# Kernel optimization log

Measured on AMD Instinct MI355X. Metric: run time of the kernel, lower is better.

The kernel has to match this reference:

```python
import jax, jax.numpy as jnp
import numpy as np

B, S = 64, 256
VOCAB, DL, DA, DV = 30522, 300, 74, 35
DH, GH, LH, RH = 128, 64, 128, 128  # modality dim, proj-GRU hidden, LSTM hidden, RGN hidden


def _gru_dir(x, Wi, Wh, bi, bh):
    # x: [B,S,D] -> [B,S,H]; torch GRU gate order (r, z, n)
    xg = x @ Wi + bi  # [B,S,3H] precomputed input projections
    H = Wh.shape[0]
    def step(h, xg_t):
        hg = h @ Wh + bh
        xr, xz, xn = jnp.split(xg_t, 3, axis=-1)
        hr, hz, hn = jnp.split(hg, 3, axis=-1)
        r = jax.nn.sigmoid(xr + hr)
        z = jax.nn.sigmoid(xz + hz)
        n = jnp.tanh(xn + r * hn)
        h = (1.0 - z) * n + z * h
        return h, h
    h0 = jnp.zeros((x.shape[0], H), x.dtype)
    _, ys = jax.lax.scan(step, h0, jnp.swapaxes(xg, 0, 1))
    return jnp.swapaxes(ys, 0, 1)


def _bigru(x, Wi, Wh, bi, bh):
    f = _gru_dir(x, Wi[0], Wh[0], bi[0], bh[0])
    b = _gru_dir(x[:, ::-1], Wi[1], Wh[1], bi[1], bh[1])[:, ::-1]
    return jnp.concatenate([f, b], axis=-1)


def _lstm_dir(x, Wi, Wh, bi, bh):
    xg = x @ Wi + bi  # [B,S,4H]; torch LSTM gate order (i, f, g, o)
    H = Wh.shape[0]
    def step(carry, xg_t):
        h, c = carry
        g = xg_t + h @ Wh + bh
        i, f, gg, o = jnp.split(g, 4, axis=-1)
        c = jax.nn.sigmoid(f) * c + jax.nn.sigmoid(i) * jnp.tanh(gg)
        h = jax.nn.sigmoid(o) * jnp.tanh(c)
        return (h, c), h
    z = jnp.zeros((x.shape[0], H), x.dtype)
    _, ys = jax.lax.scan(step, (z, z), jnp.swapaxes(xg, 0, 1))
    return jnp.swapaxes(ys, 0, 1)


def _bilstm(x, Wi, Wh, bi, bh):
    f = _lstm_dir(x, Wi[0], Wh[0], bi[0], bh[0])
    b = _lstm_dir(x[:, ::-1], Wi[1], Wh[1], bi[1], bh[1])[:, ::-1]
    return jnp.concatenate([f, b], axis=-1)


def _rgn_scan(x, h0, Wx, Wh, b):
    # RGNCell: gated recurrent cell (GRU-style), returns final state [B,H]
    xg = x @ Wx + b  # [B,S,3H]
    def step(h, xg_t):
        hg = h @ Wh
        xr, xz, xn = jnp.split(xg_t, 3, axis=-1)
        hr, hz, hn = jnp.split(hg, 3, axis=-1)
        r = jax.nn.sigmoid(xr + hr)
        z = jax.nn.sigmoid(xz + hz)
        n = jnp.tanh(xn + r * hn)
        return (1.0 - z) * n + z * h, None
    h, _ = jax.lax.scan(step, h0, jnp.swapaxes(xg, 0, 1))
    return h


def _xattn(q, kv):
    # parameter-free scaled dot-product cross-modal attention (JCAF)
    scale = 1.0 / np.sqrt(q.shape[-1]).astype(np.float32)
    s = jnp.einsum('bsd,btd->bst', q, kv) * scale
    return jnp.einsum('bst,btd->bsd', jax.nn.softmax(s, axis=-1), kv)


def _forward(sentences, acoustic, video, state0, state1, emb,
             proj_l_W, proj_l_b, proj_a_W, proj_a_b, proj_v_W, proj_v_b,
             gru_Wi, gru_Wh, gru_bi, gru_bh,
             lstm_Wi, lstm_Wh, lstm_bi, lstm_bh,
             rgn_Wx, rgn_Wh, rgn_b, fc1_W, fc1_b, fc2_W, fc2_b):
    enc = emb[sentences]                          # LanguageEmbeddingLayer: [B,S,DL]
    # SeqEncoder: project each modality to 128-d (dropout off in eval)
    seq_l = enc @ proj_l_W + proj_l_b             # [B,S,128]
    seq_a = acoustic @ proj_a_W + proj_a_b
    seq_v = video @ proj_v_W + proj_v_b
    # project_l/a/v: bidirectional GRU 128 -> 2*64 = 128
    x_l = _bigru(seq_l, gru_Wi[0], gru_Wh[0], gru_bi[0], gru_bh[0])
    x_a = _bigru(seq_a, gru_Wi[1], gru_Wh[1], gru_bi[1], gru_bh[1])
    x_v = _bigru(seq_v, gru_Wi[2], gru_Wh[2], gru_bi[2], gru_bh[2])
    # JCAF: each modality enriched by cross-attention to the other two
    fin_txt = x_l + _xattn(x_l, x_a) + _xattn(x_l, x_v)
    fin_aud = x_a + _xattn(x_a, x_l) + _xattn(x_a, x_v)
    fin_vis = x_v + _xattn(x_v, x_l) + _xattn(x_v, x_a)
    tstep = jnp.concatenate([fin_txt, fin_aud, fin_vis], axis=-1)      # [B,S,384]
    step_fusion = _bilstm(tstep, lstm_Wi, lstm_Wh, lstm_bi, lstm_bh)   # [B,S,256]
    # two custom RGNCell recurrences: forward sweep + reversed sweep
    out0 = _rgn_scan(step_fusion, state0, rgn_Wx[0], rgn_Wh[0], rgn_b[0])
    out1 = _rgn_scan(step_fusion[:, ::-1], state1, rgn_Wx[1], rgn_Wh[1], rgn_b[1])
    h = jax.nn.leaky_relu((out0 + out1) @ fc1_W + fc1_b)
    return h @ fc2_W + fc2_b                     # [B,1]


def setup_inputs():
    keys = iter(jax.random.split(jax.random.key(0), 48))
    def rn(shape, s=0.05):
        return jax.random.normal(next(keys), shape, jnp.float32) * s
    return {
        'sentences': jax.random.randint(next(keys), (B, S), 0, VOCAB),
        'acoustic': jax.random.normal(next(keys), (B, S, DA), jnp.float32),
        'video': jax.random.normal(next(keys), (B, S, DV), jnp.float32),
        'state0': jax.random.normal(next(keys), (B, RH), jnp.float32),
        'state1': jax.random.normal(next(keys), (B, RH), jnp.float32),
        'emb': rn((VOCAB, DL), 0.1),
        'proj_l_W': rn((DL, DH)), 'proj_l_b': rn((DH,)),
        'proj_a_W': rn((DA, DH)), 'proj_a_b': rn((DH,)),
        'proj_v_W': rn((DV, DH)), 'proj_v_b': rn((DH,)),
        'gru_Wi': rn((3, 2, DH, 3 * GH)), 'gru_Wh': rn((3, 2, GH, 3 * GH)),
        'gru_bi': rn((3, 2, 3 * GH)), 'gru_bh': rn((3, 2, 3 * GH)),
        'lstm_Wi': rn((2, 3 * DH, 4 * LH)), 'lstm_Wh': rn((2, LH, 4 * LH)),
        'lstm_bi': rn((2, 4 * LH)), 'lstm_bh': rn((2, 4 * LH)),
        'rgn_Wx': rn((2, 2 * LH, 3 * RH)), 'rgn_Wh': rn((2, RH, 3 * RH)),
        'rgn_b': rn((2, 3 * RH)),
        'fc1_W': rn((RH, 32)), 'fc1_b': rn((32,)),
        'fc2_W': rn((32, 1)), 'fc2_b': rn((1,)),
    }


def reference(sentences, acoustic, video, state0, state1, emb,
              proj_l_W, proj_l_b, proj_a_W, proj_a_b, proj_v_W, proj_v_b,
              gru_Wi, gru_Wh, gru_bi, gru_bh,
              lstm_Wi, lstm_Wh, lstm_bi, lstm_bh,
              rgn_Wx, rgn_Wh, rgn_b, fc1_W, fc1_b, fc2_W, fc2_b):
    return _forward(sentences, acoustic, video, state0, state1, emb,
                    proj_l_W, proj_l_b, proj_a_W, proj_a_b, proj_v_W, proj_v_b,
                    gru_Wi, gru_Wh, gru_bi, gru_bh,
                    lstm_Wi, lstm_Wh, lstm_bi, lstm_bh,
                    rgn_Wx, rgn_Wh, rgn_b, fc1_W, fc1_b, fc2_W, fc2_b)
```

## Files before the change

### kernel.cpp

```cpp
#include <hip/hip_runtime.h>

#define WS_SEQ      0LL
#define WS_XGGRU    6291456LL
#define WS_X        0LL
#define WS_TSTEP    18874368LL
#define WS_S        6291456LL
#define WS_XGLSTM   0LL
#define WS_SF       16777216LL
#define WS_XGRGN    0LL
#define WS_OUT0     20971520LL

__device__ __forceinline__ float sigf(float x) {
    return __builtin_amdgcn_rcpf(1.f + __expf(-x));
}
__device__ __forceinline__ float tanhfast(float x) {
    float e = __expf(2.f * x);
    return 1.f - 2.f * __builtin_amdgcn_rcpf(e + 1.f);
}

typedef float vf2 __attribute__((ext_vector_type(2)));

#define LDW64(W, P, S) { _Pragma("unroll") \
    for (int _k = 0; _k < 64; ++_k) (W)[_k] = *(const vf2*)((P) + _k * (S)); }

#define PK4(A0, A1, Wa, Wb, Wc, Wd, H, K0, K1, K2, K3) \
  asm("v_readlane_b32 s60, %6, " #K0 "\n\t" \
      "v_readlane_b32 s62, %6, " #K1 "\n\t" \
      "v_readlane_b32 s64, %6, " #K2 "\n\t" \
      "v_readlane_b32 s66, %6, " #K3 "\n\t" \
      "s_mov_b32 s61, s60\n\t" \
      "s_mov_b32 s63, s62\n\t" \
      "s_mov_b32 s65, s64\n\t" \
      "s_mov_b32 s67, s66\n\t" \
      "v_pk_fma_f32 %0, %2, s[60:61], %0\n\t" \
      "v_pk_fma_f32 %1, %3, s[62:63], %1\n\t" \
      "v_pk_fma_f32 %0, %4, s[64:65], %0\n\t" \
      "v_pk_fma_f32 %1, %5, s[66:67], %1" \
      : "+v"(A0), "+v"(A1) \
      : "v"(Wa), "v"(Wb), "v"(Wc), "v"(Wd), "v"(H) \
      : "s60","s61","s62","s63","s64","s65","s66","s67");

#define PKALL(A0, A1, W, H) \
  PK4(A0,A1,W[0],W[1],W[2],W[3],H,0,1,2,3) \
  PK4(A0,A1,W[4],W[5],W[6],W[7],H,4,5,6,7) \
  PK4(A0,A1,W[8],W[9],W[10],W[11],H,8,9,10,11) \
  PK4(A0,A1,W[12],W[13],W[14],W[15],H,12,13,14,15) \
  PK4(A0,A1,W[16],W[17],W[18],W[19],H,16,17,18,19) \
  PK4(A0,A1,W[20],W[21],W[22],W[23],H,20,21,22,23) \
  PK4(A0,A1,W[24],W[25],W[26],W[27],H,24,25,26,27) \
  PK4(A0,A1,W[28],W[29],W[30],W[31],H,28,29,30,31) \
  PK4(A0,A1,W[32],W[33],W[34],W[35],H,32,33,34,35) \
  PK4(A0,A1,W[36],W[37],W[38],W[39],H,36,37,38,39) \
  PK4(A0,A1,W[40],W[41],W[42],W[43],H,40,41,42,43) \
  PK4(A0,A1,W[44],W[45],W[46],W[47],H,44,45,46,47) \
  PK4(A0,A1,W[48],W[49],W[50],W[51],H,48,49,50,51) \
  PK4(A0,A1,W[52],W[53],W[54],W[55],H,52,53,54,55) \
  PK4(A0,A1,W[56],W[57],W[58],W[59],H,56,57,58,59) \
  PK4(A0,A1,W[60],W[61],W[62],W[63],H,60,61,62,63)

__device__ __forceinline__ void gemm_body(
    const float* __restrict__ Ab, int lda, const int* __restrict__ idx,
    const float* __restrict__ Wb, int wld, int wtrans,
    const float* __restrict__ bb,
    float* __restrict__ Cb, int ldc,
    int K, float alpha, int accum)
{
    int m0 = blockIdx.y * 64, n0 = blockIdx.x * 64;
    int t = threadIdx.x;
    int tx = t & 7, ty = t >> 3;

    __shared__ __align__(16) float As[16][68];
    __shared__ __align__(16) float Ws[16][68];

    float acc[8][8];
#pragma unroll
    for (int i = 0; i < 8; ++i)
#pragma unroll
        for (int j = 0; j < 8; ++j) acc[i][j] = 0.f;

    long long arow[4];
#pragma unroll
    for (int i = 0; i < 4; ++i) {
        int m = (t + i * 64) >> 2;
        arow[i] = idx ? (long long)idx[m0 + m] : (long long)(m0 + m);
    }
    const bool a_vec = ((lda & 3) == 0);

    for (int k0 = 0; k0 < K; k0 += 16) {
#pragma unroll
        for (int i = 0; i < 4; ++i) {
            int j = t + i * 64;
            int m = j >> 2, kq = j & 3;
            int kk = k0 + kq * 4;
            const float* p = Ab + arow[i] * (long long)lda + kk;
            float4 v = {0.f, 0.f, 0.f, 0.f};
            if (a_vec && kk + 3 < K) {
                v = *(const float4*)p;
            } else {
                if (kk + 0 < K) v.x = p[0];
                if (kk + 1 < K) v.y = p[1];
                if (kk + 2 < K) v.z = p[2];
                if (kk + 3 < K) v.w = p[3];
            }
            As[kq * 4 + 0][m] = v.x; As[kq * 4 + 1][m] = v.y;
            As[kq * 4 + 2][m] = v.z; As[kq * 4 + 3][m] = v.w;
        }
        if (!wtrans) {
#pragma unroll
            for (int i = 0; i < 4; ++i) {
                int j = t + i * 64;
                int k = j >> 4, nq = j & 15;
                float4 v = {0.f, 0.f, 0.f, 0.f};
                if (k0 + k < K)
                    v = *(const float4*)(Wb + (long long)(k0 + k) * wld + n0 + nq * 4);
                *(float4*)&Ws[k][nq * 4] = v;
            }
        } else {
#pragma unroll
            for (int i = 0; i < 4; ++i) {
                int j = t + i * 64;
                int n = j >> 2, kq = j & 3;
                int kk = k0 + kq * 4;
                const float* p = Wb + (long long)(n0 + n) * wld + kk;
                float4 v = {0.f, 0.f, 0.f, 0.f};
                if (kk + 3 < K) v = *(const float4*)p;
                else {
                    if (kk + 0 < K) v.x = p[0];
                    if (kk + 1 < K) v.y = p[1];
                    if (kk + 2 < K) v.z = p[2];
                    if (kk + 3 < K) v.w = p[3];
                }
                Ws[kq * 4 + 0][n] = v.x; Ws[kq * 4 + 1][n] = v.y;
                Ws[kq * 4 + 2][n] = v.z; Ws[kq * 4 + 3][n] = v.w;
            }
        }
        __syncthreads();
#pragma unroll
        for (int k = 0; k < 16; ++k) {
            float4 a0 = *(const float4*)&As[k][ty * 8];
            float4 a1 = *(const float4*)&As[k][ty * 8 + 4];
            float4 b0 = *(const float4*)&Ws[k][tx * 8];
            float4 b1 = *(const float4*)&Ws[k][tx * 8 + 4];
            float av[8] = {a0.x, a0.y, a0.z, a0.w, a1.x, a1.y, a1.z, a1.w};
            float bv[8] = {b0.x, b0.y, b0.z, b0.w, b1.x, b1.y, b1.z, b1.w};
#pragma unroll
            for (int i = 0; i < 8; ++i)
#pragma unroll
                for (int j = 0; j < 8; ++j)
                    acc[i][j] = fmaf(av[i], bv[j], acc[i][j]);
        }
        __syncthreads();
    }

#pragma unroll
    for (int i = 0; i < 8; ++i) {
        long long gm = m0 + ty * 8 + i;
#pragma unroll
        for (int jq = 0; jq < 2; ++jq) {
            float* cp = Cb + gm * ldc + n0 + tx * 8 + jq * 4;
            float4 v;
            v.x = alpha * acc[i][jq * 4 + 0]; v.y = alpha * acc[i][jq * 4 + 1];
            v.z = alpha * acc[i][jq * 4 + 2]; v.w = alpha * acc[i][jq * 4 + 3];
            if (bb) {
                const float* bp = bb + n0 + tx * 8 + jq * 4;
                v.x += bp[0]; v.y += bp[1]; v.z += bp[2]; v.w += bp[3];
            }
            if (accum) {
                float4 o = *(const float4*)cp;
                v.x += o.x; v.y += o.y; v.z += o.z; v.w += o.w;
            }
            *(float4*)cp = v;
        }
    }
}

__global__ __launch_bounds__(64) void gemm_k(
    const float* __restrict__ A, long long a_z, int a_zdiv, int lda,
    const int* __restrict__ idx,
    const float* __restrict__ W, long long w_z, int wld, int wtrans,
    const float* __restrict__ bias, int bias_z,
    float* __restrict__ C, long long c_z, int ldc,
    int K, float alpha, int accum)
{
    int z = blockIdx.z;
    gemm_body(A + (long long)(z / a_zdiv) * a_z, lda, idx,
              W + (long long)z * w_z, wld, wtrans,
              bias ? bias + (long long)z * bias_z : nullptr,
              C + (long long)z * c_z, ldc, K, alpha, accum);
}

__global__ __launch_bounds__(64) void att_score_k(
    const float* __restrict__ X, float* __restrict__ S,
    int q0, int q1, int q2, int k0, int k1, int k2)
{
    int z = blockIdx.z;
    int pair = z >> 6, b = z & 63;
    int qi = pair == 0 ? q0 : (pair == 1 ? q1 : q2);
    int ki = pair == 0 ? k0 : (pair == 1 ? k1 : k2);
    gemm_body(X + (long long)qi * 2097152 + (long long)b * 32768, 128, nullptr,
              X + (long long)ki * 2097152 + (long long)b * 32768, 128, 1,
              nullptr,
              S + (long long)z * 65536, 256, 128, 0.08838834764831845f, 0);
}

__global__ __launch_bounds__(64) void att_apply_k(
    const float* __restrict__ S, const float* __restrict__ X,
    float* __restrict__ tstep,
    int q0, int q1, int q2, int k0, int k1, int k2)
{
    int z = blockIdx.z;
    int pair = z >> 6, b = z & 63;
    int qi = pair == 0 ? q0 : (pair == 1 ? q1 : q2);
    int ki = pair == 0 ? k0 : (pair == 1 ? k1 : k2);
    gemm_body(S + (long long)z * 65536, 256, nullptr,
              X + (long long)ki * 2097152 + (long long)b * 32768, 128, 0,
              nullptr,
              tstep + (long long)qi * 128 + (long long)b * 98304, 384,
              256, 1.f, 1);
}

__global__ __launch_bounds__(256) void copy_tstep_k(const float* __restrict__ x,
                                                    float* __restrict__ tstep)
{
    int o = blockIdx.x * 256 + threadIdx.x;
    int c = o % 384;
    int row = o / 384;
    int m = c >> 7, cc = c & 127;
    tstep[o] = x[(long long)m * 2097152 + (long long)row * 128 + cc];
}

__global__ __launch_bounds__(256) void softmax_k(float* __restrict__ S)
{
    int wave = threadIdx.x >> 6, lane = threadIdx.x & 63;
    int row = blockIdx.x * 4 + wave;
    float* p = S + (long long)row * 256;
    float v[4];
    float mx = -1e30f;
#pragma unroll
    for (int i = 0; i < 4; ++i) { v[i] = p[lane + i * 64]; mx = fmaxf(mx, v[i]); }
#pragma unroll
    for (int off = 32; off > 0; off >>= 1) mx = fmaxf(mx, __shfl_xor(mx, off));
    float sum = 0.f;
#pragma unroll
    for (int i = 0; i < 4; ++i) { v[i] = __expf(v[i] - mx); sum += v[i]; }
#pragma unroll
    for (int off = 32; off > 0; off >>= 1) sum += __shfl_xor(sum, off);
    float inv = 1.f / sum;
#pragma unroll
    for (int i = 0; i < 4; ++i) p[lane + i * 64] = v[i] * inv;
}

__global__ __launch_bounds__(128) void gru_rec_k(const float* __restrict__ xg,
                                                 const float* __restrict__ Wh,
                                                 const float* __restrict__ bh,
                                                 float* __restrict__ xout)
{
    int b = blockIdx.x, z = blockIdx.y;
    int m = z >> 1, d = z & 1;
    int tid = threadIdx.x, lane = tid & 63;
    int cp = tid;
    int act = cp < 96;
    int cpc = act ? cp : 0;
    const float* Whz = Wh + (long long)z * 12288;
    const float* wp = Whz + 2 * cpc;
    vf2 Wk[64];
    LDW64(Wk, wp, 192);
    vf2 bias2 = *(const vf2*)(bh + z * 192 + 2 * cpc);

    __shared__ float g[2][192];
    int n = lane;
    float h = 0.f;
    const float* xgb = xg + (long long)z * 3145728 + (long long)b * 49152;
    float* xob = xout + (long long)m * 2097152 + (long long)b * 32768 + d * 64;
    int tt0 = d ? 255 : 0;
    const float* xr0 = xgb + tt0 * 192;
    float x_r = xr0[n], x_z = xr0[64 + n], x_n = xr0[128 + n];

#pragma unroll 1
    for (int t = 0; t < 256; ++t) {
        int tt = d ? 255 - t : t;
        float nx_r = 0, nx_z = 0, nx_n = 0;
        if (t < 255) {
            const float* xr = xgb + (d ? tt - 1 : tt + 1) * 192;
            nx_r = xr[n]; nx_z = xr[64 + n]; nx_n = xr[128 + n];
        }
        vf2 a0 = bias2, a1 = {0.f, 0.f};
        PKALL(a0, a1, Wk, h);
        if (act) *(vf2*)&g[t & 1][2 * cp] = a0 + a1;
        __syncthreads();
        const float* gp = g[t & 1];
        float r  = sigf(x_r + gp[n]);
        float zz = sigf(x_z + gp[64 + n]);
        float nn = tanhfast(x_n + r * gp[128 + n]);
        h = (1.f - zz) * nn + zz * h;
        if (tid < 64) xob[tt * 128 + n] = h;
        x_r = nx_r; x_z = nx_z; x_n = nx_n;
    }
}

__global__ __launch_bounds__(512) void lstm_rec_k(const float* __restrict__ xg,
                                                  const float* __restrict__ Wh,
                                                  const float* __restrict__ bh,
                                                  float* __restrict__ sf)
{
    int b = blockIdx.x, d = blockIdx.y;
    int tid = threadIdx.x, lane = tid & 63;
    int kh = tid >> 8;
    int cp = tid & 255;
    const float* Whz = Wh + (long long)d * 65536;
    const float* wp = Whz + (long long)(kh * 64) * 512 + 2 * cp;
    vf2 Wk[64];
    LDW64(Wk, wp, 512);

    __shared__ float part[2][1024];
    int n = kh * 64 + lane;
    float h = 0.f, cst = 0.f;
    const float* xgb = xg + (long long)d * 8388608 + (long long)b * 131072;
    float* sfb = sf + (long long)b * 65536 + d * 128;

    vf2 bias2 = {0.f, 0.f}, xc2 = {0.f, 0.f};
    if (kh == 0) {
        bias2 = *(const vf2*)(bh + d * 512 + 2 * cp);
        int tt0 = d ? 255 : 0;
        xc2 = *(const vf2*)(xgb + tt0 * 512 + 2 * cp);
    }

#pragma unroll 1
    for (int t = 0; t < 256; ++t) {
        int tt = d ? 255 - t : t;
        vf2 nxc2 = {0.f, 0.f};
        if (kh == 0 && t < 255)
            nxc2 = *(const vf2*)(xgb + (d ? tt - 1 : tt + 1) * 512 + 2 * cp);
        vf2 a0 = xc2 + bias2, a1 = {0.f, 0.f};
        PKALL(a0, a1, Wk, h);
        *(vf2*)&part[t & 1][kh * 512 + 2 * cp] = a0 + a1;
        __syncthreads();
        const float* p = part[t & 1];
        float iv = p[n]       + p[512 + n];
        float fv = p[128 + n] + p[512 + 128 + n];
        float gv = p[256 + n] + p[512 + 256 + n];
        float ov = p[384 + n] + p[512 + 384 + n];
        cst = sigf(fv) * cst + sigf(iv) * tanhfast(gv);
        h = sigf(ov) * tanhfast(cst);
        if (cp < 64) sfb[tt * 256 + n] = h;
        xc2 = nxc2;
    }
}

__global__ __launch_bounds__(384) void rgn_rec_k(const float* __restrict__ xg,
                                                 const float* __restrict__ Wh,
                                                 const float* __restrict__ state0,
                                                 const float* __restrict__ state1,
                                                 float* __restrict__ outbase)
{
    int b = blockIdx.x, d = blockIdx.y;
    int tid = threadIdx.x, lane = tid & 63;
    int kh = (tid >= 192) ? 1 : 0;
    int cp = tid - kh * 192;
    const float* Whz = Wh + (long long)d * 49152;
    const float* wp = Whz + (long long)(kh * 64) * 384 + 2 * cp;
    vf2 Wk[64];
    LDW64(Wk, wp, 384);

    __shared__ float part[2][768];
    int n = kh * 64 + lane;
    const float* st = d ? state1 : state0;
    float h = st[b * 128 + n];
    const float* xgb = xg + (long long)d * 6291456 + (long long)b * 98304;
    int tt0 = d ? 255 : 0;
    const float* xr0 = xgb + tt0 * 384;
    float x_r = xr0[n], x_z = xr0[128 + n], x_n = xr0[256 + n];

#pragma unroll 1
    for (int t = 0; t < 256; ++t) {
        int tt = d ? 255 - t : t;
        float nx_r = 0, nx_z = 0, nx_n = 0;
        if (t < 255) {
            const float* xr = xgb + (d ? tt - 1 : tt + 1) * 384;
            nx_r = xr[n]; nx_z = xr[128 + n]; nx_n = xr[256 + n];
        }
        vf2 a0 = {0.f, 0.f}, a1 = {0.f, 0.f};
        PKALL(a0, a1, Wk, h);
        *(vf2*)&part[t & 1][kh * 384 + 2 * cp] = a0 + a1;
        __syncthreads();
        const float* p = part[t & 1];
        float pr = p[n]       + p[384 + n];
        float pz = p[128 + n] + p[384 + 128 + n];
        float pn = p[256 + n] + p[384 + 256 + n];
        float r  = sigf(x_r + pr);
        float zz = sigf(x_z + pz);
        float nn = tanhfast(x_n + r * pn);
        h = (1.f - zz) * nn + zz * h;
        x_r = nx_r; x_z = nx_z; x_n = nx_n;
    }
    if (cp < 64) outbase[(long long)d * 8192 + b * 128 + n] = h;
}

__global__ __launch_bounds__(256) void fc_k(const float* __restrict__ o01,
                                            const float* __restrict__ f1W,
                                            const float* __restrict__ f1b,
                                            const float* __restrict__ f2W,
                                            const float* __restrict__ f2b,
                                            float* __restrict__ out)
{
    __shared__ float s[8192];
    __shared__ float h1[2048];
    int tid = threadIdx.x;
    for (int e = tid; e < 8192; e += 256) s[e] = o01[e] + o01[8192 + e];
    __syncthreads();
    for (int o = tid; o < 2048; o += 256) {
        int b = o >> 5, q = o & 31;
        float acc = f1b[q];
        for (int k = 0; k < 128; ++k) acc += s[b * 128 + k] * f1W[k * 32 + q];
        h1[o] = acc >= 0.f ? acc : 0.01f * acc;
    }
    __syncthreads();
    if (tid < 64) {
        float acc = f2b[0];
        for (int q = 0; q < 32; ++q) acc += h1[tid * 32 + q] * f2W[q];
        out[tid] = acc;
    }
}

extern "C" void kernel_launch(void* const* d_in, const int* in_sizes, int n_in,
                              void* d_out, int out_size, void* d_ws, size_t ws_size,
                              hipStream_t stream)
{
    const int*   sent     = (const int*)  d_in[0];
    const float* acoustic = (const float*)d_in[1];
    const float* video    = (const float*)d_in[2];
    const float* state0   = (const float*)d_in[3];
    const float* state1   = (const float*)d_in[4];
    const float* emb      = (const float*)d_in[5];
    const float* plW = (const float*)d_in[6],  *plb = (const float*)d_in[7];
    const float* paW = (const float*)d_in[8],  *pab = (const float*)d_in[9];
    const float* pvW = (const float*)d_in[10], *pvb = (const float*)d_in[11];
    const float* gWi = (const float*)d_in[12], *gWh = (const float*)d_in[13];
    const float* gbi = (const float*)d_in[14], *gbh = (const float*)d_in[15];
    const float* lWi = (const float*)d_in[16], *lWh = (const float*)d_in[17];
    const float* lbi = (const float*)d_in[18], *lbh = (const float*)d_in[19];
    const float* rWx = (const float*)d_in[20], *rWh = (const float*)d_in[21];
    const float* rb  = (const float*)d_in[22];
    const float* f1W = (const float*)d_in[23], *f1b = (const float*)d_in[24];
    const float* f2W = (const float*)d_in[25], *f2b = (const float*)d_in[26];
    float* ws  = (float*)d_ws;
    float* out = (float*)d_out;

    dim3 blk(64);

    gemm_k<<<dim3(2, 256, 1), blk, 0, stream>>>(emb, 0, 1, 300, sent,
        plW, 0, 128, 0, plb, 0, ws + WS_SEQ, 0, 128, 300, 1.f, 0);
    gemm_k<<<dim3(2, 256, 1), blk, 0, stream>>>(acoustic, 0, 1, 74, nullptr,
        paW, 0, 128, 0, pab, 0, ws + WS_SEQ + 2097152, 0, 128, 74, 1.f, 0);
    gemm_k<<<dim3(2, 256, 1), blk, 0, stream>>>(video, 0, 1, 35, nullptr,
        pvW, 0, 128, 0, pvb, 0, ws + WS_SEQ + 4194304, 0, 128, 35, 1.f, 0);

    gemm_k<<<dim3(3, 256, 6), blk, 0, stream>>>(ws + WS_SEQ, 2097152, 2, 128, nullptr,
        gWi, 24576, 192, 0, gbi, 192, ws + WS_XGGRU, 3145728, 192, 128, 1.f, 0);

    gru_rec_k<<<dim3(64, 6), dim3(128), 0, stream>>>(ws + WS_XGGRU, gWh, gbh, ws + WS_X);

    copy_tstep_k<<<dim3(24576), dim3(256), 0, stream>>>(ws + WS_X, ws + WS_TSTEP);

    att_score_k<<<dim3(4, 4, 192), blk, 0, stream>>>(ws + WS_X, ws + WS_S,
        0, 1, 2, 1, 0, 0);
    softmax_k<<<dim3(12288), dim3(256), 0, stream>>>(ws + WS_S);
    att_apply_k<<<dim3(2, 4, 192), blk, 0, stream>>>(ws + WS_S, ws + WS_X,
        ws + WS_TSTEP, 0, 1, 2, 1, 0, 0);
    att_score_k<<<dim3(4, 4, 192), blk, 0, stream>>>(ws + WS_X, ws + WS_S,
        0, 1, 2, 2, 2, 1);
    softmax_k<<<dim3(12288), dim3(256), 0, stream>>>(ws + WS_S);
    att_apply_k<<<dim3(2, 4, 192), blk, 0, stream>>>(ws + WS_S, ws + WS_X,
        ws + WS_TSTEP, 0, 1, 2, 2, 2, 1);

    gemm_k<<<dim3(8, 256, 2), blk, 0, stream>>>(ws + WS_TSTEP, 0, 1, 384, nullptr,
        lWi, 196608, 512, 0, lbi, 512, ws + WS_XGLSTM, 8388608, 512, 384, 1.f, 0);

    lstm_rec_k<<<dim3(64, 2), dim3(512), 0, stream>>>(ws + WS_XGLSTM, lWh, lbh, ws + WS_SF);

    gemm_k<<<dim3(6, 256, 2), blk, 0, stream>>>(ws + WS_SF, 0, 1, 256, nullptr,
        rWx, 98304, 384, 0, rb, 384, ws + WS_XGRGN, 6291456, 384, 256, 1.f, 0);

    rgn_rec_k<<<dim3(64, 2), dim3(384), 0, stream>>>(ws + WS_XGRGN, rWh, state0, state1,
                                                     ws + WS_OUT0);

    fc_k<<<dim3(1), dim3(256), 0, stream>>>(ws + WS_OUT0, f1W, f1b, f2W, f2b, out);
}
```

Measured before the change: 1.729 ms.

## Split recurrent matvec K dimension across more waves in GRU/LSTM/RGN kernels

Each recurrent kernel (GRU, LSTM, RGN) now splits the hidden-state reduction into 32-element K chunks across twice as many threads. Each thread holds 32 instead of 64 weight pairs in registers, pinned with an empty asm. Partial sums are written to shared memory in a [col][kq] layout so the reduction reads them back as one float4. This shortens the serial per-step FMA chain, the critical path of the 256-step recurrences, at the cost of more threads per block, extra shared-memory reduction work and larger barriers.

```diff
diff --git a/kernel.cpp b/kernel.cpp
--- a/kernel.cpp
+++ b/kernel.cpp
@@ -20,8 +20,10 @@
 
 typedef float vf2 __attribute__((ext_vector_type(2)));
 
-#define LDW64(W, P, S) { _Pragma("unroll") \
-    for (int _k = 0; _k < 64; ++_k) (W)[_k] = *(const vf2*)((P) + _k * (S)); }
+#define LDW32_PIN(W, P, S) { _Pragma("unroll") \
+    for (int _k = 0; _k < 32; ++_k) { \
+        (W)[_k] = *(const vf2*)((P) + _k * (S)); \
+        asm("" : "+v"((W)[_k])); } }
 
 #define PK4(A0, A1, Wa, Wb, Wc, Wd, H, K0, K1, K2, K3) \
   asm("v_readlane_b32 s60, %6, " #K0 "\n\t" \
@@ -40,7 +42,7 @@
       : "v"(Wa), "v"(Wb), "v"(Wc), "v"(Wd), "v"(H) \
       : "s60","s61","s62","s63","s64","s65","s66","s67");
 
-#define PKALL(A0, A1, W, H) \
+#define PKALL32(A0, A1, W, H) \
   PK4(A0,A1,W[0],W[1],W[2],W[3],H,0,1,2,3) \
   PK4(A0,A1,W[4],W[5],W[6],W[7],H,4,5,6,7) \
   PK4(A0,A1,W[8],W[9],W[10],W[11],H,8,9,10,11) \
@@ -48,15 +50,7 @@
   PK4(A0,A1,W[16],W[17],W[18],W[19],H,16,17,18,19) \
   PK4(A0,A1,W[20],W[21],W[22],W[23],H,20,21,22,23) \
   PK4(A0,A1,W[24],W[25],W[26],W[27],H,24,25,26,27) \
-  PK4(A0,A1,W[28],W[29],W[30],W[31],H,28,29,30,31) \
-  PK4(A0,A1,W[32],W[33],W[34],W[35],H,32,33,34,35) \
-  PK4(A0,A1,W[36],W[37],W[38],W[39],H,36,37,38,39) \
-  PK4(A0,A1,W[40],W[41],W[42],W[43],H,40,41,42,43) \
-  PK4(A0,A1,W[44],W[45],W[46],W[47],H,44,45,46,47) \
-  PK4(A0,A1,W[48],W[49],W[50],W[51],H,48,49,50,51) \
-  PK4(A0,A1,W[52],W[53],W[54],W[55],H,52,53,54,55) \
-  PK4(A0,A1,W[56],W[57],W[58],W[59],H,56,57,58,59) \
-  PK4(A0,A1,W[60],W[61],W[62],W[63],H,60,61,62,63)
+  PK4(A0,A1,W[28],W[29],W[30],W[31],H,28,29,30,31)
 
 __device__ __forceinline__ void gemm_body(
     const float* __restrict__ Ab, int lda, const int* __restrict__ idx,
@@ -250,25 +244,27 @@
     for (int i = 0; i < 4; ++i) p[lane + i * 64] = v[i] * inv;
 }
 
-__global__ __launch_bounds__(128) void gru_rec_k(const float* __restrict__ xg,
-                                                 const float* __restrict__ Wh,
-                                                 const float* __restrict__ bh,
-                                                 float* __restrict__ xout)
+__global__ __launch_bounds__(256, 4) void gru_rec_k(const float* __restrict__ xg,
+                                                    const float* __restrict__ Wh,
+                                                    const float* __restrict__ bh,
+                                                    float* __restrict__ xout)
 {
     int b = blockIdx.x, z = blockIdx.y;
     int m = z >> 1, d = z & 1;
     int tid = threadIdx.x, lane = tid & 63;
-    int cp = tid;
+    int kq = tid >> 7;
+    int cp = tid & 127;
     int act = cp < 96;
     int cpc = act ? cp : 0;
     const float* Whz = Wh + (long long)z * 12288;
-    const float* wp = Whz + 2 * cpc;
-    vf2 Wk[64];
-    LDW64(Wk, wp, 192);
-    vf2 bias2 = *(const vf2*)(bh + z * 192 + 2 * cpc);
-
-    __shared__ float g[2][192];
-    int n = lane;
+    const float* wp = Whz + (long long)(kq * 32) * 192 + 2 * cpc;
+    vf2 Wk[32];
+    LDW32_PIN(Wk, wp, 192);
+    vf2 bias2 = {0.f, 0.f};
+    if (kq == 0) bias2 = *(const vf2*)(bh + z * 192 + 2 * cpc);
+
+    __shared__ float g[2][2][192];
+    int n = kq * 32 + (lane & 31);
     float h = 0.f;
     const float* xgb = xg + (long long)z * 3145728 + (long long)b * 49152;
     float* xob = xout + (long long)m * 2097152 + (long long)b * 32768 + d * 64;
@@ -285,41 +281,44 @@
             nx_r = xr[n]; nx_z = xr[64 + n]; nx_n = xr[128 + n];
         }
         vf2 a0 = bias2, a1 = {0.f, 0.f};
-        PKALL(a0, a1, Wk, h);
-        if (act) *(vf2*)&g[t & 1][2 * cp] = a0 + a1;
+        PKALL32(a0, a1, Wk, h);
+        if (act) *(vf2*)&g[t & 1][kq][2 * cp] = a0 + a1;
         __syncthreads();
-        const float* gp = g[t & 1];
-        float r  = sigf(x_r + gp[n]);
-        float zz = sigf(x_z + gp[64 + n]);
-        float nn = tanhfast(x_n + r * gp[128 + n]);
+        const float* gp = &g[t & 1][0][0];
+        float pr = gp[n]       + gp[192 + n];
+        float pz = gp[64 + n]  + gp[192 + 64 + n];
+        float pn = gp[128 + n] + gp[192 + 128 + n];
+        float r  = sigf(x_r + pr);
+        float zz = sigf(x_z + pz);
+        float nn = tanhfast(x_n + r * pn);
         h = (1.f - zz) * nn + zz * h;
-        if (tid < 64) xob[tt * 128 + n] = h;
+        if (cp < 32) xob[tt * 128 + n] = h;
         x_r = nx_r; x_z = nx_z; x_n = nx_n;
     }
 }
 
-__global__ __launch_bounds__(512) void lstm_rec_k(const float* __restrict__ xg,
-                                                  const float* __restrict__ Wh,
-                                                  const float* __restrict__ bh,
-                                                  float* __restrict__ sf)
+__global__ __launch_bounds__(1024, 4) void lstm_rec_k(const float* __restrict__ xg,
+                                                      const float* __restrict__ Wh,
+                                                      const float* __restrict__ bh,
+                                                      float* __restrict__ sf)
 {
     int b = blockIdx.x, d = blockIdx.y;
     int tid = threadIdx.x, lane = tid & 63;
-    int kh = tid >> 8;
+    int kq = tid >> 8;
     int cp = tid & 255;
     const float* Whz = Wh + (long long)d * 65536;
-    const float* wp = Whz + (long long)(kh * 64) * 512 + 2 * cp;
-    vf2 Wk[64];
-    LDW64(Wk, wp, 512);
-
-    __shared__ float part[2][1024];
-    int n = kh * 64 + lane;
+    const float* wp = Whz + (long long)(kq * 32) * 512 + 2 * cp;
+    vf2 Wk[32];
+    LDW32_PIN(Wk, wp, 512);
+
+    __shared__ __align__(16) float part[2][512][4];
+    int n = kq * 32 + (lane & 31);
     float h = 0.f, cst = 0.f;
     const float* xgb = xg + (long long)d * 8388608 + (long long)b * 131072;
     float* sfb = sf + (long long)b * 65536 + d * 128;
 
     vf2 bias2 = {0.f, 0.f}, xc2 = {0.f, 0.f};
-    if (kh == 0) {
+    if (kq == 0) {
         bias2 = *(const vf2*)(bh + d * 512 + 2 * cp);
         int tt0 = d ? 255 : 0;
         xc2 = *(const vf2*)(xgb + tt0 * 512 + 2 * cp);
@@ -329,41 +328,44 @@
     for (int t = 0; t < 256; ++t) {
         int tt = d ? 255 - t : t;
         vf2 nxc2 = {0.f, 0.f};
-        if (kh == 0 && t < 255)
+        if (kq == 0 && t < 255)
             nxc2 = *(const vf2*)(xgb + (d ? tt - 1 : tt + 1) * 512 + 2 * cp);
         vf2 a0 = xc2 + bias2, a1 = {0.f, 0.f};
-        PKALL(a0, a1, Wk, h);
-        *(vf2*)&part[t & 1][kh * 512 + 2 * cp] = a0 + a1;
+        PKALL32(a0, a1, Wk, h);
+        vf2 s = a0 + a1;
+        part[t & 1][2 * cp][kq] = s.x;
+        part[t & 1][2 * cp + 1][kq] = s.y;
         __syncthreads();
-        const float* p = part[t & 1];
-        float iv = p[n]       + p[512 + n];
-        float fv = p[128 + n] + p[512 + 128 + n];
-        float gv = p[256 + n] + p[512 + 256 + n];
-        float ov = p[384 + n] + p[512 + 384 + n];
+        const float4* p4 = (const float4*)&part[t & 1][0][0];
+        float4 vi = p4[n], vf = p4[128 + n], vg = p4[256 + n], vo = p4[384 + n];
+        float iv = (vi.x + vi.y) + (vi.z + vi.w);
+        float fv = (vf.x + vf.y) + (vf.z + vf.w);
+        float gv = (vg.x + vg.y) + (vg.z + vg.w);
+        float ov = (vo.x + vo.y) + (vo.z + vo.w);
         cst = sigf(fv) * cst + sigf(iv) * tanhfast(gv);
         h = sigf(ov) * tanhfast(cst);
-        if (cp < 64) sfb[tt * 256 + n] = h;
+        if (cp < 32) sfb[tt * 256 + n] = h;
         xc2 = nxc2;
     }
 }
 
-__global__ __launch_bounds__(384) void rgn_rec_k(const float* __restrict__ xg,
-                                                 const float* __restrict__ Wh,
-                                                 const float* __restrict__ state0,
-                                                 const float* __restrict__ state1,
-                                                 float* __restrict__ outbase)
+__global__ __launch_bounds__(768, 3) void rgn_rec_k(const float* __restrict__ xg,
+                                                    const float* __restrict__ Wh,
+                                                    const float* __restrict__ state0,
+                                                    const float* __restrict__ state1,
+                                                    float* __restrict__ outbase)
 {
     int b = blockIdx.x, d = blockIdx.y;
     int tid = threadIdx.x, lane = tid & 63;
-    int kh = (tid >= 192) ? 1 : 0;
-    int cp = tid - kh * 192;
+    int kq = tid / 192;
+    int cp = tid - kq * 192;
     const float* Whz = Wh + (long long)d * 49152;
-    const float* wp = Whz + (long long)(kh * 64) * 384 + 2 * cp;
-    vf2 Wk[64];
-    LDW64(Wk, wp, 384);
-
-    __shared__ float part[2][768];
-    int n = kh * 64 + lane;
+    const float* wp = Whz + (long long)(kq * 32) * 384 + 2 * cp;
+    vf2 Wk[32];
+    LDW32_PIN(Wk, wp, 384);
+
+    __shared__ __align__(16) float part[2][384][4];
+    int n = kq * 32 + (lane & 31);
     const float* st = d ? state1 : state0;
     float h = st[b * 128 + n];
     const float* xgb = xg + (long long)d * 6291456 + (long long)b * 98304;
@@ -380,20 +382,23 @@
             nx_r = xr[n]; nx_z = xr[128 + n]; nx_n = xr[256 + n];
         }
         vf2 a0 = {0.f, 0.f}, a1 = {0.f, 0.f};
-        PKALL(a0, a1, Wk, h);
-        *(vf2*)&part[t & 1][kh * 384 + 2 * cp] = a0 + a1;
+        PKALL32(a0, a1, Wk, h);
+        vf2 s = a0 + a1;
+        part[t & 1][2 * cp][kq] = s.x;
+        part[t & 1][2 * cp + 1][kq] = s.y;
         __syncthreads();
-        const float* p = part[t & 1];
-        float pr = p[n]       + p[384 + n];
-        float pz = p[128 + n] + p[384 + 128 + n];
-        float pn = p[256 + n] + p[384 + 256 + n];
+        const float4* p4 = (const float4*)&part[t & 1][0][0];
+        float4 vr = p4[n], vz = p4[128 + n], vn = p4[256 + n];
+        float pr = (vr.x + vr.y) + (vr.z + vr.w);
+        float pz = (vz.x + vz.y) + (vz.z + vz.w);
+        float pn = (vn.x + vn.y) + (vn.z + vn.w);
         float r  = sigf(x_r + pr);
         float zz = sigf(x_z + pz);
         float nn = tanhfast(x_n + r * pn);
         h = (1.f - zz) * nn + zz * h;
         x_r = nx_r; x_z = nx_z; x_n = nx_n;
     }
-    if (cp < 64) outbase[(long long)d * 8192 + b * 128 + n] = h;
+    if (cp < 32) outbase[(long long)d * 8192 + b * 128 + n] = h;
 }
 
 __global__ __launch_bounds__(256) void fc_k(const float* __restrict__ o01,
@@ -458,7 +463,7 @@
     gemm_k<<<dim3(3, 256, 6), blk, 0, stream>>>(ws + WS_SEQ, 2097152, 2, 128, nullptr,
         gWi, 24576, 192, 0, gbi, 192, ws + WS_XGGRU, 3145728, 192, 128, 1.f, 0);
 
-    gru_rec_k<<<dim3(64, 6), dim3(128), 0, stream>>>(ws + WS_XGGRU, gWh, gbh, ws + WS_X);
+    gru_rec_k<<<dim3(64, 6), dim3(256), 0, stream>>>(ws + WS_XGGRU, gWh, gbh, ws + WS_X);
 
     copy_tstep_k<<<dim3(24576), dim3(256), 0, stream>>>(ws + WS_X, ws + WS_TSTEP);
 
@@ -476,12 +481,12 @@
     gemm_k<<<dim3(8, 256, 2), blk, 0, stream>>>(ws + WS_TSTEP, 0, 1, 384, nullptr,
         lWi, 196608, 512, 0, lbi, 512, ws + WS_XGLSTM, 8388608, 512, 384, 1.f, 0);
 
-    lstm_rec_k<<<dim3(64, 2), dim3(512), 0, stream>>>(ws + WS_XGLSTM, lWh, lbh, ws + WS_SF);
+    lstm_rec_k<<<dim3(64, 2), dim3(1024), 0, stream>>>(ws + WS_XGLSTM, lWh, lbh, ws + WS_SF);
 
     gemm_k<<<dim3(6, 256, 2), blk, 0, stream>>>(ws + WS_SF, 0, 1, 256, nullptr,
         rWx, 98304, 384, 0, rb, 384, ws + WS_XGRGN, 6291456, 384, 256, 1.f, 0);
 
-    rgn_rec_k<<<dim3(64, 2), dim3(384), 0, stream>>>(ws + WS_XGRGN, rWh, state0, state1,
+    rgn_rec_k<<<dim3(64, 2), dim3(768), 0, stream>>>(ws + WS_XGRGN, rWh, state0, state1,
                                                      ws + WS_OUT0);
 
     fc_k<<<dim3(1), dim3(256), 0, stream>>>(ws + WS_OUT0, f1W, f1b, f2W, f2b, out);
```

After: 1.701 ms. About the same (-1.6%).

## Use one column per thread in GRU/RGN recurrences and packed FMA in GEMM

Applied to the files above, without the earlier changes.

The GRU and RGN recurrent kernels now give each thread a single output column instead of two, which doubles the thread count per block (192 and 768). Each thread does scalar readlane-broadcast FMAs split across four independent accumulators in place of the inline-asm packed FMA chains. The goal is to shorten the serial per-step dot-product latency by spreading it over more threads, at the cost of more waves per block and more readlane instructions. Separately, the tiled GEMM inner loop is rewritten to use two-wide vector FMA accumulators so the compiler can emit packed FP32 FMAs.

```diff
diff --git a/kernel.cpp b/kernel.cpp
--- a/kernel.cpp
+++ b/kernel.cpp
@@ -17,8 +17,17 @@
     float e = __expf(2.f * x);
     return 1.f - 2.f * __builtin_amdgcn_rcpf(e + 1.f);
 }
-
+__device__ __forceinline__ float rl(float v, int i) {
+    return __int_as_float(__builtin_amdgcn_readlane(__float_as_int(v), i));
+}
+
+typedef float vf16 __attribute__((ext_vector_type(16)));
 typedef float vf2 __attribute__((ext_vector_type(2)));
+
+#define LD16(V, P, S) { _Pragma("unroll") \
+    for (int _j = 0; _j < 16; ++_j) (V)[_j] = (P)[_j * (S)]; }
+#define DOT16(ACC, V, H, B) { _Pragma("unroll") \
+    for (int _j = 0; _j < 16; ++_j) (ACC) = fmaf(rl((H), (B) + _j), (V)[_j], (ACC)); }
 
 #define LDW64(W, P, S) { _Pragma("unroll") \
     for (int _k = 0; _k < 64; ++_k) (W)[_k] = *(const vf2*)((P) + _k * (S)); }
@@ -72,11 +81,11 @@
     __shared__ __align__(16) float As[16][68];
     __shared__ __align__(16) float Ws[16][68];
 
-    float acc[8][8];
+    vf2 acc2[8][4];
 #pragma unroll
     for (int i = 0; i < 8; ++i)
 #pragma unroll
-        for (int j = 0; j < 8; ++j) acc[i][j] = 0.f;
+        for (int j = 0; j < 4; ++j) acc2[i][j] = (vf2){0.f, 0.f};
 
     long long arow[4];
 #pragma unroll
@@ -142,12 +151,16 @@
             float4 b0 = *(const float4*)&Ws[k][tx * 8];
             float4 b1 = *(const float4*)&Ws[k][tx * 8 + 4];
             float av[8] = {a0.x, a0.y, a0.z, a0.w, a1.x, a1.y, a1.z, a1.w};
-            float bv[8] = {b0.x, b0.y, b0.z, b0.w, b1.x, b1.y, b1.z, b1.w};
-#pragma unroll
-            for (int i = 0; i < 8; ++i)
-#pragma unroll
-                for (int j = 0; j < 8; ++j)
-                    acc[i][j] = fmaf(av[i], bv[j], acc[i][j]);
+            vf2 bv[4];
+            bv[0] = (vf2){b0.x, b0.y}; bv[1] = (vf2){b0.z, b0.w};
+            bv[2] = (vf2){b1.x, b1.y}; bv[3] = (vf2){b1.z, b1.w};
+#pragma unroll
+            for (int i = 0; i < 8; ++i) {
+                vf2 a2 = {av[i], av[i]};
+#pragma unroll
+                for (int j = 0; j < 4; ++j)
+                    acc2[i][j] = __builtin_elementwise_fma(a2, bv[j], acc2[i][j]);
+            }
         }
         __syncthreads();
     }
@@ -159,8 +172,10 @@
         for (int jq = 0; jq < 2; ++jq) {
             float* cp = Cb + gm * ldc + n0 + tx * 8 + jq * 4;
             float4 v;
-            v.x = alpha * acc[i][jq * 4 + 0]; v.y = alpha * acc[i][jq * 4 + 1];
-            v.z = alpha * acc[i][jq * 4 + 2]; v.w = alpha * acc[i][jq * 4 + 3];
+            v.x = alpha * acc2[i][jq * 2 + 0][0];
+            v.y = alpha * acc2[i][jq * 2 + 0][1];
+            v.z = alpha * acc2[i][jq * 2 + 1][0];
+            v.w = alpha * acc2[i][jq * 2 + 1][1];
             if (bb) {
                 const float* bp = bb + n0 + tx * 8 + jq * 4;
                 v.x += bp[0]; v.y += bp[1]; v.z += bp[2]; v.w += bp[3];
@@ -250,7 +265,7 @@
     for (int i = 0; i < 4; ++i) p[lane + i * 64] = v[i] * inv;
 }
 
-__global__ __launch_bounds__(128) void gru_rec_k(const float* __restrict__ xg,
+__global__ __launch_bounds__(192) void gru_rec_k(const float* __restrict__ xg,
                                                  const float* __restrict__ Wh,
                                                  const float* __restrict__ bh,
                                                  float* __restrict__ xout)
@@ -258,14 +273,13 @@
     int b = blockIdx.x, z = blockIdx.y;
     int m = z >> 1, d = z & 1;
     int tid = threadIdx.x, lane = tid & 63;
-    int cp = tid;
-    int act = cp < 96;
-    int cpc = act ? cp : 0;
+    int c = tid;
     const float* Whz = Wh + (long long)z * 12288;
-    const float* wp = Whz + 2 * cpc;
-    vf2 Wk[64];
-    LDW64(Wk, wp, 192);
-    vf2 bias2 = *(const vf2*)(bh + z * 192 + 2 * cpc);
+    const float* wp = Whz + c;
+    vf16 W0, W1, W2, W3;
+    LD16(W0, wp + 0 * 16 * 192, 192); LD16(W1, wp + 1 * 16 * 192, 192);
+    LD16(W2, wp + 2 * 16 * 192, 192); LD16(W3, wp + 3 * 16 * 192, 192);
+    float bias = bh[z * 192 + c];
 
     __shared__ float g[2][192];
     int n = lane;
@@ -284,16 +298,17 @@
             const float* xr = xgb + (d ? tt - 1 : tt + 1) * 192;
             nx_r = xr[n]; nx_z = xr[64 + n]; nx_n = xr[128 + n];
         }
-        vf2 a0 = bias2, a1 = {0.f, 0.f};
-        PKALL(a0, a1, Wk, h);
-        if (act) *(vf2*)&g[t & 1][2 * cp] = a0 + a1;
+        float s0 = bias, s1 = 0.f, s2 = 0.f, s3 = 0.f;
+        DOT16(s0, W0, h, 0);  DOT16(s1, W1, h, 16);
+        DOT16(s2, W2, h, 32); DOT16(s3, W3, h, 48);
+        g[t & 1][c] = (s0 + s1) + (s2 + s3);
         __syncthreads();
         const float* gp = g[t & 1];
         float r  = sigf(x_r + gp[n]);
         float zz = sigf(x_z + gp[64 + n]);
         float nn = tanhfast(x_n + r * gp[128 + n]);
         h = (1.f - zz) * nn + zz * h;
-        if (tid < 64) xob[tt * 128 + n] = h;
+        if (c < 64) xob[tt * 128 + n] = h;
         x_r = nx_r; x_z = nx_z; x_n = nx_n;
     }
 }
@@ -347,7 +362,7 @@
     }
 }
 
-__global__ __launch_bounds__(384) void rgn_rec_k(const float* __restrict__ xg,
+__global__ __launch_bounds__(768) void rgn_rec_k(const float* __restrict__ xg,
                                                  const float* __restrict__ Wh,
                                                  const float* __restrict__ state0,
                                                  const float* __restrict__ state1,
@@ -355,12 +370,13 @@
 {
     int b = blockIdx.x, d = blockIdx.y;
     int tid = threadIdx.x, lane = tid & 63;
-    int kh = (tid >= 192) ? 1 : 0;
-    int cp = tid - kh * 192;
+    int kh = (tid >= 384) ? 1 : 0;
+    int c  = tid - kh * 384;
     const float* Whz = Wh + (long long)d * 49152;
-    const float* wp = Whz + (long long)(kh * 64) * 384 + 2 * cp;
-    vf2 Wk[64];
-    LDW64(Wk, wp, 384);
+    const float* wp = Whz + (long long)(kh * 64) * 384 + c;
+    vf16 W0, W1, W2, W3;
+    LD16(W0, wp + 0 * 16 * 384, 384); LD16(W1, wp + 1 * 16 * 384, 384);
+    LD16(W2, wp + 2 * 16 * 384, 384); LD16(W3, wp + 3 * 16 * 384, 384);
 
     __shared__ float part[2][768];
     int n = kh * 64 + lane;
@@ -379,9 +395,10 @@
             const float* xr = xgb + (d ? tt - 1 : tt + 1) * 384;
             nx_r = xr[n]; nx_z = xr[128 + n]; nx_n = xr[256 + n];
         }
-        vf2 a0 = {0.f, 0.f}, a1 = {0.f, 0.f};
-        PKALL(a0, a1, Wk, h);
-        *(vf2*)&part[t & 1][kh * 384 + 2 * cp] = a0 + a1;
+        float s0 = 0.f, s1 = 0.f, s2 = 0.f, s3 = 0.f;
+        DOT16(s0, W0, h, 0);  DOT16(s1, W1, h, 16);
+        DOT16(s2, W2, h, 32); DOT16(s3, W3, h, 48);
+        part[t & 1][kh * 384 + c] = (s0 + s1) + (s2 + s3);
         __syncthreads();
         const float* p = part[t & 1];
         float pr = p[n]       + p[384 + n];
@@ -393,7 +410,7 @@
         h = (1.f - zz) * nn + zz * h;
         x_r = nx_r; x_z = nx_z; x_n = nx_n;
     }
-    if (cp < 64) outbase[(long long)d * 8192 + b * 128 + n] = h;
+    if (c < 64) outbase[(long long)d * 8192 + b * 128 + n] = h;
 }
 
 __global__ __launch_bounds__(256) void fc_k(const float* __restrict__ o01,
@@ -458,7 +475,7 @@
     gemm_k<<<dim3(3, 256, 6), blk, 0, stream>>>(ws + WS_SEQ, 2097152, 2, 128, nullptr,
         gWi, 24576, 192, 0, gbi, 192, ws + WS_XGGRU, 3145728, 192, 128, 1.f, 0);
 
-    gru_rec_k<<<dim3(64, 6), dim3(128), 0, stream>>>(ws + WS_XGGRU, gWh, gbh, ws + WS_X);
+    gru_rec_k<<<dim3(64, 6), dim3(192), 0, stream>>>(ws + WS_XGGRU, gWh, gbh, ws + WS_X);
 
     copy_tstep_k<<<dim3(24576), dim3(256), 0, stream>>>(ws + WS_X, ws + WS_TSTEP);
 
@@ -481,7 +498,7 @@
     gemm_k<<<dim3(6, 256, 2), blk, 0, stream>>>(ws + WS_SF, 0, 1, 256, nullptr,
         rWx, 98304, 384, 0, rb, 384, ws + WS_XGRGN, 6291456, 384, 256, 1.f, 0);
 
-    rgn_rec_k<<<dim3(64, 2), dim3(384), 0, stream>>>(ws + WS_XGRGN, rWh, state0, state1,
+    rgn_rec_k<<<dim3(64, 2), dim3(768), 0, stream>>>(ws + WS_XGRGN, rWh, state0, state1,
                                                      ws + WS_OUT0);
 
     fc_k<<<dim3(1), dim3(256), 0, stream>>>(ws + WS_OUT0, f1W, f1b, f2W, f2b, out);
```

After: 1.579 ms. 1.09x faster.
